# Kernel optimization log

Hardware: AMD Instinct MI355X
Metric: run time of the kernel (lower is better)

Reference implementation:

```python
import jax, jax.numpy as jnp
import numpy as np

B = 256          # graphs per batch
NN = 400         # ROI nodes per graph (N*(N-1)/2 = 79800 = input_dim)
HID = [32, 64, 128]
KS = [200, 100, 50]   # nodes kept after each TopKPooling (ratio 0.5 each)
EPS = 1e-5


def setup_inputs() -> dict:
    key = jax.random.key(0)
    ks = jax.random.split(key, 20)
    # flattened strict upper triangle of a nonnegative FC matrix per sample
    data = jax.random.uniform(ks[0], (B, NN * (NN - 1) // 2), dtype=jnp.float32)
    inp = {"data": data}
    dims = [1] + HID
    for l in range(3):
        fan_in = dims[l]
        inp[f"W{l+1}"] = jax.random.normal(ks[1 + 5 * l], (dims[l], dims[l + 1]), jnp.float32) / np.sqrt(fan_in)
        inp[f"b{l+1}"] = jnp.zeros((dims[l + 1],), jnp.float32)
        inp[f"g{l+1}"] = jnp.ones((dims[l + 1],), jnp.float32)      # BN gamma
        inp[f"be{l+1}"] = jnp.zeros((dims[l + 1],), jnp.float32)    # BN beta
        inp[f"p{l+1}"] = jax.random.normal(ks[4 + 5 * l], (dims[l + 1],), jnp.float32) * 0.1  # TopK score vector
    return inp


def _gcn_conv(A, X, W, b):
    # GCNConv with edge weights: add self loops (weight 1), symmetric D^-1/2 A D^-1/2
    n = A.shape[1]
    Al = A + jnp.eye(n, dtype=A.dtype)[None]          # (B, n, n)
    deg = Al.sum(axis=-1)                             # (B, n)
    dis = jnp.where(deg > 0, jax.lax.rsqrt(deg), 0.0)
    An = dis[:, :, None] * Al * dis[:, None, :]
    return jnp.einsum('bij,bjf->bif', An, X @ W) + b


def _block(A, X, W, b, g, be, p, k):
    # GCNConv -> ReLU -> BatchNorm(train stats) -> (dropout=identity) -> TopKPooling
    h = jax.nn.relu(_gcn_conv(A, X, W, b))
    mu = h.mean(axis=(0, 1))
    var = h.var(axis=(0, 1))
    h = (h - mu) * jax.lax.rsqrt(var + EPS) * g + be
    # TopKPooling: score = x . p / ||p||, keep top k per graph, gate by tanh(score)
    score = h @ p / jnp.linalg.norm(p)                # (B, n)
    vals, idx = jax.lax.top_k(score, k)               # (B, k)
    Xn = jnp.take_along_axis(h, idx[:, :, None], axis=1) * jnp.tanh(vals)[:, :, None]
    bi = jnp.arange(A.shape[0])[:, None, None]
    An = A[bi, idx[:, :, None], idx[:, None, :]]      # filter_adj: edges among kept nodes
    return An, Xn


def reference(data, W1, b1, g1, be1, p1, W2, b2, g2, be2, p2, W3, b3, g3, be3, p3):
    Bn = data.shape[0]
    iu0, iu1 = np.triu_indices(NN, 1)
    A = jnp.zeros((Bn, NN, NN), data.dtype).at[:, iu0, iu1].set(data)
    A = A + jnp.swapaxes(A, 1, 2)                     # symmetric FC adjacency, zero diag
    X = jnp.ones((Bn, NN, 1), data.dtype)             # initial node feature dim = 1
    A, X = _block(A, X, W1, b1, g1, be1, p1, KS[0])
    A, X = _block(A, X, W2, b2, g2, be2, p2, KS[1])
    A, X = _block(A, X, W3, b3, g3, be3, p3, KS[2])
    return X.max(axis=1)                              # global_max_pool -> (B, 128)
```

## Files before the change

kernel.cpp:

```cpp
#include <hip/hip_runtime.h>
#include <math.h>

#define BB   256
#define NN0  400
#define NE   79800
#define EPSF 1e-5f

__device__ __forceinline__ int tri_e(int a, int c) {
  return a*(NN0-1) - ((a*(a-1))>>1) + (c - a - 1);
}

__device__ __forceinline__ size_t PRI(int b, int ti, int tj, int r) {
  return (((size_t)b*7 + ti)*7 + tj)*64 + r;
}

__device__ __forceinline__ float wave_sum(float v) {
  #pragma unroll
  for (int o = 32; o > 0; o >>= 1) v += __shfl_xor(v, o, 64);
  return v;
}

__device__ __forceinline__ const float* lane0_ptr(const float* p) {
  uint64_t v = (uint64_t)p;
  uint32_t lo = (uint32_t)__builtin_amdgcn_readfirstlane((int)(v & 0xffffffffu));
  uint32_t hi = (uint32_t)__builtin_amdgcn_readfirstlane((int)(v >> 32));
  return (const float*)((((uint64_t)hi) << 32) | lo);
}

__device__ __forceinline__ void bitonic_desc(float* sc, int* si, int P) {
  const int tid = threadIdx.x;
  const int nt = blockDim.x;
  for (int k = 2; k <= P; k <<= 1) {
    for (int j = k >> 1; j > 0; j >>= 1) {
      __syncthreads();
      for (int i = tid; i < P; i += nt) {
        int ixj = i ^ j;
        if (ixj > i) {
          float a = sc[i], c = sc[ixj];
          int ai = si[i], ci = si[ixj];
          bool bef = (a > c) || (a == c && ai < ci);
          bool sw = ((i & k) == 0) ? !bef : bef;
          if (sw) { sc[i] = c; sc[ixj] = a; si[i] = ci; si[ixj] = ai; }
        }
      }
    }
  }
  __syncthreads();
}

__global__ __launch_bounds__(256) void k_tri_mv(
    const float* __restrict__ data,
    const float* __restrict__ pr_in, const float* __restrict__ pc_in,
    float* __restrict__ pr, float* __restrict__ pc) {
  __shared__ float tile[64][65];
  __shared__ float dI[64], dJ[64];
  const int xcd = blockIdx.x & 7, slot = blockIdx.x >> 3;
  const int b = xcd*32 + slot/7, q0 = slot % 7;
  const int tid = threadIdx.x;
  const int wave = tid >> 6, lane = tid & 63;
  const float* __restrict__ drow = data + (size_t)b*NE;
  int ti_a[4], tj_a[4];
  #pragma unroll
  for (int u = 0; u < 4; ++u) {
    int t = q0 + u*7;
    int ti = 0, rem = t;
    while (rem >= 7 - ti) { rem -= 7 - ti; ++ti; }
    ti_a[u] = ti; tj_a[u] = ti + rem;
  }
  float vreg[16];
  float rI = 0.f, rJ = 0.f;
  auto issue = [&](int u) {
    const int i0 = ti_a[u]*64, j0 = tj_a[u]*64;
    const int ni = min(64, NN0 - i0), nj = min(64, NN0 - j0);
    #pragma unroll
    for (int k = 0; k < 16; ++k) {
      const int rr = wave*16 + k;
      const int i = i0 + rr, j = j0 + lane;
      vreg[k] = 0.f;
      if (rr < ni && lane < nj && j > i) vreg[k] = drow[tri_e(i, j)];
    }
    if (pr_in) {
      if (tid < 64) {
        float a = 0.f;
        if (tid < ni) {
          const int tt = ti_a[u], r = tid;
          float acc = 1.f;
          for (int tj = tt; tj < 7; ++tj) acc += pr_in[PRI(b, tt, tj, r)];
          for (int ts = 0; ts <= tt; ++ts) acc += pc_in[PRI(b, ts, tt, r)];
          a = rsqrtf(acc);
        }
        rI = a;
      } else if (tid < 128) {
        const int c = tid - 64;
        float a = 0.f;
        if (c < nj) {
          const int tt = tj_a[u], r = c;
          float acc = 1.f;
          for (int tj = tt; tj < 7; ++tj) acc += pr_in[PRI(b, tt, tj, r)];
          for (int ts = 0; ts <= tt; ++ts) acc += pc_in[PRI(b, ts, tt, r)];
          a = rsqrtf(acc);
        }
        rJ = a;
      }
    } else {
      if (tid < 64) rI = (tid < ni) ? 1.f : 0.f;
      else if (tid < 128) rJ = (tid - 64 < nj) ? 1.f : 0.f;
    }
  };
  issue(0);
  #pragma unroll 1
  for (int u = 0; u < 4; ++u) {
    const int ti = ti_a[u], tj = tj_a[u];
    if (u) __syncthreads();
    #pragma unroll
    for (int k = 0; k < 16; ++k) tile[wave*16 + k][lane] = vreg[k];
    if (tid < 64) dI[tid] = rI;
    else if (tid < 128) dJ[tid-64] = rJ;
    __syncthreads();
    if (u + 1 < 4) issue(u + 1);
    {
      const int r = tid >> 2, q = tid & 3;
      float s = 0.f;
      #pragma unroll
      for (int c = 0; c < 16; ++c) s += tile[r][q*16 + c] * dJ[q*16 + c];
      s += __shfl_xor(s, 1, 64);
      s += __shfl_xor(s, 2, 64);
      if (q == 0) pr[PRI(b, ti, tj, r)] = s;
    }
    {
      const int c = tid >> 2, q = tid & 3;
      float s = 0.f;
      #pragma unroll
      for (int r = 0; r < 16; ++r) s += tile[q*16 + r][c] * dI[q*16 + r];
      s += __shfl_xor(s, 1, 64);
      s += __shfl_xor(s, 2, 64);
      if (q == 0) pc[PRI(b, ti, tj, c)] = s;
    }
  }
}

__global__ __launch_bounds__(256) void k_sfin_stats_red(
    const float* __restrict__ pr, const float* __restrict__ pc,
    const float* __restrict__ pr2, const float* __restrict__ pc2,
    const float* __restrict__ W1, const float* __restrict__ b1,
    float* __restrict__ s1, float* __restrict__ acc1) {
  __shared__ float sl[256];
  __shared__ float st[64];
  __shared__ float w1s[32], b1s[32];
  const int tid = threadIdx.x;
  const int i = blockIdx.x*256 + tid;
  if (tid < 32) { w1s[tid] = W1[tid]; b1s[tid] = b1[tid]; }
  if (tid < 64) st[tid] = 0.f;
  const int b = i / NN0, n = i % NN0;
  const int t = n >> 6, r = n & 63;
  float dacc = 1.f, sacc = 0.f;
  for (int tj = t; tj < 7; ++tj) { dacc += pr[PRI(b, t, tj, r)]; sacc += pr2[PRI(b, t, tj, r)]; }
  for (int ti = 0; ti <= t; ++ti) { dacc += pc[PRI(b, ti, t, r)]; sacc += pc2[PRI(b, ti, t, r)]; }
  const float d = rsqrtf(dacc);
  const float s = d * (d + sacc);
  s1[i] = s;
  sl[tid] = s;
  __syncthreads();
  const int f = tid & 31, sub = tid >> 5;
  const float w = w1s[f], bb = b1s[f];
  float S = 0.f, Q = 0.f;
  #pragma unroll
  for (int k = 0; k < 32; ++k) {
    const float ss = sl[sub*32 + k];
    const float h = fmaxf(ss*w + bb, 0.f);
    S += h; Q += h*h;
  }
  atomicAdd(&st[f], S);
  atomicAdd(&st[32+f], Q);
  __syncthreads();
  if (tid < 64) atomicAdd(&acc1[tid], st[tid]);
}

__global__ __launch_bounds__(512) void k_top1(
    const float* __restrict__ s1, const float* __restrict__ acc1,
    const float* __restrict__ W1, const float* __restrict__ b1,
    const float* __restrict__ g1, const float* __restrict__ be1,
    const float* __restrict__ p1, const float* __restrict__ W2,
    int* __restrict__ nodes2, int* __restrict__ sperm2, float* __restrict__ Y2) {
  __shared__ float sc[512]; __shared__ int si[512];
  __shared__ float sS[NN0];
  __shared__ float tvs[200];
  __shared__ int nds_l[200];
  __shared__ float w1s[32], b1s[32], cfs[32], scs[32], shs[32];
  __shared__ __align__(16) float hp[6400];
  __shared__ float c0s;
  const int tid = threadIdx.x;
  const int b = (blockIdx.x & 7)*32 + (blockIdx.x >> 3);
  if (tid < 32) { w1s[tid] = W1[tid]; b1s[tid] = b1[tid]; }
  if (tid < 64) {
    float scale = 0.f, shift = 0.f, pv = 0.f;
    if (tid < 32) {
      const float S = acc1[tid], Q = acc1[32 + tid];
      const float N = 102400.f;
      const float mu = S / N;
      const float var = Q / N - mu*mu;
      const float inv = rsqrtf(var + EPSF);
      scale = inv * g1[tid];
      shift = be1[tid] - mu * scale;
      pv = p1[tid];
    }
    const float pn = sqrtf(wave_sum(pv*pv));
    if (tid < 32) { scs[tid] = scale; shs[tid] = shift; cfs[tid] = scale*pv/pn; }
    float u = (tid < 32) ? shift*pv/pn : 0.f;
    u = wave_sum(u);
    if (tid == 0) c0s = u;
  }
  __syncthreads();
  const float c0 = c0s;
  {
    const int i = tid;
    if (i < NN0) {
      const float s = s1[(size_t)b*NN0 + i];
      sS[i] = s;
      float sco = c0;
      #pragma unroll
      for (int f = 0; f < 32; ++f) sco += fmaxf(s*w1s[f] + b1s[f], 0.f) * cfs[f];
      sc[i] = sco; si[i] = i;
    } else { sc[i] = -INFINITY; si[i] = 0x7fffffff; }
  }
  bitonic_desc(sc, si, 512);
  for (int k = tid; k < 200; k += 512) {
    tvs[k] = tanhf(sc[k]);
    nds_l[k] = si[k];
    nodes2[b*200 + k] = si[k];
  }
  __syncthreads();
  for (int o = tid; o < 6400; o += 512) {
    const int k = o >> 5, f = o & 31;
    const float s = sS[nds_l[k]];
    const float h = fmaxf(s*w1s[f] + b1s[f], 0.f);
    hp[o] = (h*scs[f] + shs[f]) * tvs[k];
  }
  __syncthreads();
  {
    const int g = tid & 63;
    float wr[32];
    #pragma unroll
    for (int f = 0; f < 32; ++f) wr[f] = W2[f*64 + g];
    for (int o = tid; o < 12800; o += 512) {
      const int k = o >> 6;
      float acc = 0.f;
      #pragma unroll
      for (int c4 = 0; c4 < 8; ++c4) {
        const float4 x4 = *(const float4*)&hp[(k<<5) + (c4<<2)];
        acc += x4.x*wr[c4*4] + x4.y*wr[c4*4+1] + x4.z*wr[c4*4+2] + x4.w*wr[c4*4+3];
      }
      Y2[(size_t)b*12800 + o] = acc;
    }
  }
  __syncthreads();
  if (tid < 256) {
    sc[tid] = (tid < 200) ? -(float)nds_l[tid] : -INFINITY;
    si[tid] = (tid < 200) ? tid : 0x7fffffff;
  }
  bitonic_desc(sc, si, 256);
  if (tid < 200) sperm2[b*200 + tid] = si[tid];
}

__global__ __launch_bounds__(256) void k_gatherA2(
    const float* __restrict__ data, const int* __restrict__ nodes2,
    const int* __restrict__ sperm2, float* __restrict__ A2, float* __restrict__ dis2) {
  __shared__ int nds[200], sp[200], sn[200];
  __shared__ float rowbuf[4][200];
  const int idx = blockIdx.x;
  const int r9 = idx >> 3;
  const int b = (idx & 7)*32 + r9/50;
  const int rg = r9 % 50;
  const int tid = threadIdx.x;
  if (tid < 200) { nds[tid] = nodes2[b*200 + tid]; sp[tid] = sperm2[b*200 + tid]; }
  __syncthreads();
  if (tid < 200) sn[tid] = nds[sp[tid]];
  __syncthreads();
  const int wave = tid >> 6, lane = tid & 63;
  const int i = rg*4 + wave;
  const int ni = nds[i];
  const float* __restrict__ drow = data + (size_t)b*NE;
  float accd = 0.f;
  for (int jj = lane; jj < 200; jj += 64) {
    const int sj = sn[jj];
    float v = 0.f;
    if (sj != ni) {
      const int a = min(ni, sj), c = max(ni, sj);
      v = drow[tri_e(a, c)];
    }
    rowbuf[wave][sp[jj]] = v;
    accd += v;
  }
  __syncthreads();
  accd = wave_sum(accd);
  const float dd = rsqrtf(1.f + accd);
  for (int j = lane; j < 200; j += 64)
    A2[((size_t)b*200 + i)*200 + j] = rowbuf[wave][j] * dd;
  if (lane == 0) dis2[b*200 + i] = dd;
}

__global__ __launch_bounds__(256) void k_conv2(
    const float* __restrict__ A2, const float* __restrict__ Y2,
    const float* __restrict__ dis2, const float* __restrict__ b2,
    float* __restrict__ h2g, float* __restrict__ acc2g) {
  __shared__ float dsb[200];
  __shared__ float st[128];
  const int tid = threadIdx.x;
  const int xcd = blockIdx.x & 7, slot = blockIdx.x >> 3;
  const int b = xcd*32 + slot/5, p = slot % 5;
  const int wave = tid >> 6, lane = tid & 63;
  if (tid < 128) st[tid] = 0.f;
  if (tid < 200) dsb[tid] = dis2[b*200 + tid];
  __syncthreads();
  const float bl = b2[lane];
  const int rb = p*40 + wave*10;
  const float* __restrict__ Yb = Y2 + (size_t)b*12800;
  const float* __restrict__ Aw = lane0_ptr(A2 + (size_t)b*40000 + rb);
  float acc[10];
  #pragma unroll
  for (int k = 0; k < 10; ++k) acc[k] = 0.f;
  float zA = Yb[lane], zB = Yb[64 + lane];
  #pragma unroll 2
  for (int jp = 0; jp < 100; ++jp) {
    const int j = jp << 1;
    const float za = zA, zb_ = zB;
    if (jp < 99) { zA = Yb[(j + 2)*64 + lane]; zB = Yb[(j + 3)*64 + lane]; }
    const float* __restrict__ Aj0 = Aw + (size_t)j*200;
    const float* __restrict__ Aj1 = Aw + (size_t)(j + 1)*200;
    #pragma unroll
    for (int k = 0; k < 10; ++k) acc[k] = fmaf(Aj0[k], za, acc[k]);
    #pragma unroll
    for (int k = 0; k < 10; ++k) acc[k] = fmaf(Aj1[k], zb_, acc[k]);
  }
  float ss = 0.f, qq = 0.f;
  #pragma unroll
  for (int k = 0; k < 10; ++k) {
    const int r = rb + k;
    const float d = dsb[r];
    const float y = Yb[(size_t)r*64 + lane];
    const float h = fmaxf(d*acc[k] + d*(d*y) + bl, 0.f);
    h2g[((size_t)b*200 + r)*64 + lane] = h;
    ss += h; qq += h*h;
  }
  atomicAdd(&st[lane], ss);
  atomicAdd(&st[64 + lane], qq);
  __syncthreads();
  if (tid < 128) atomicAdd(&acc2g[tid], st[tid]);
}

__global__ __launch_bounds__(512) void k_top2(
    const float* __restrict__ h2g, const float* __restrict__ acc2,
    const float* __restrict__ g2, const float* __restrict__ be2,
    const float* __restrict__ p2, const float* __restrict__ W3,
    const int* __restrict__ nodes2, int* __restrict__ nodes3,
    float* __restrict__ Y3) {
  __shared__ float sc[256]; __shared__ int si[256];
  __shared__ __align__(16) float xs[6400];
  __shared__ float sc2[64], sh2[64], cf2[64];
  __shared__ float c20s;
  const int tid = threadIdx.x;
  const int b = (blockIdx.x & 7)*32 + (blockIdx.x >> 3);
  if (tid < 64) {
    const float S = acc2[tid], Q = acc2[64 + tid];
    const float N = 51200.f;
    const float mu = S/N, var = Q/N - mu*mu, inv = rsqrtf(var + EPSF);
    const float scale = inv*g2[tid], shift = be2[tid] - mu*scale;
    const float pv = p2[tid];
    const float pn = sqrtf(wave_sum(pv*pv));
    sc2[tid] = scale; sh2[tid] = shift; cf2[tid] = scale*pv/pn;
    const float u = wave_sum(shift*pv/pn);
    if (tid == 0) c20s = u;
  }
  __syncthreads();
  const int wave = tid >> 6, lane = tid & 63;
  const float cf = cf2[lane];
  const float c20 = c20s;
  for (int i = wave; i < 200; i += 8) {
    float v = h2g[((size_t)b*200 + i)*64 + lane] * cf;
    v = wave_sum(v);
    if (lane == 0) { sc[i] = v + c20; si[i] = i; }
  }
  if (tid >= 200 && tid < 256) { sc[tid] = -INFINITY; si[tid] = 0x7fffffff; }
  bitonic_desc(sc, si, 256);
  const float scale = sc2[lane], shift = sh2[lane];
  for (int o = tid; o < 6400; o += 512) {
    const int k = o >> 6;
    const int idx = si[k];
    const float tv = tanhf(sc[k]);
    xs[o] = (h2g[((size_t)b*200 + idx)*64 + lane] * scale + shift) * tv;
  }
  for (int k = tid; k < 100; k += 512) nodes3[b*100 + k] = nodes2[b*200 + si[k]];
  __syncthreads();
  {
    const int g = tid & 127;
    float wr[64];
    #pragma unroll
    for (int f = 0; f < 64; ++f) wr[f] = W3[f*128 + g];
    for (int o = tid; o < 12800; o += 512) {
      const int k = o >> 7;
      float acc = 0.f;
      #pragma unroll
      for (int c4 = 0; c4 < 16; ++c4) {
        const float4 x4 = *(const float4*)&xs[(k<<6) + (c4<<2)];
        acc += x4.x*wr[c4*4] + x4.y*wr[c4*4+1] + x4.z*wr[c4*4+2] + x4.w*wr[c4*4+3];
      }
      Y3[(size_t)b*12800 + o] = acc;
    }
  }
}

__global__ __launch_bounds__(256) void k_gatherA3(
    const float* __restrict__ data, const int* __restrict__ nodes3,
    float* __restrict__ A3, float* __restrict__ dis3) {
  __shared__ int nds[100];
  const int slot = blockIdx.x >> 3;
  const int b = (blockIdx.x & 7)*32 + slot/25, rg = slot % 25;
  const int tid = threadIdx.x;
  if (tid < 100) nds[tid] = nodes3[b*100 + tid];
  __syncthreads();
  const int wave = tid >> 6, lane = tid & 63;
  const int i = rg*4 + wave;
  const int ni = nds[i];
  const float* __restrict__ drow = data + (size_t)b*NE;
  const int j0 = lane, j1 = 64 + lane;
  float v0 = 0.f, v1 = 0.f;
  if (j0 != i) {
    const int nj = nds[j0];
    const int a = min(ni, nj), c = max(ni, nj);
    v0 = drow[tri_e(a, c)];
  }
  if (j1 < 100 && j1 != i) {
    const int nj = nds[j1];
    const int a = min(ni, nj), c = max(ni, nj);
    v1 = drow[tri_e(a, c)];
  }
  const float accd = wave_sum(v0 + v1);
  const float dd = rsqrtf(1.f + accd);
  A3[((size_t)b*100 + i)*100 + j0] = v0 * dd;
  if (j1 < 100) A3[((size_t)b*100 + i)*100 + j1] = v1 * dd;
  if (lane == 0) dis3[b*100 + i] = dd;
}

__global__ __launch_bounds__(256) void k_conv3(
    const float* __restrict__ A3, const float* __restrict__ Y3,
    const float* __restrict__ dis3, const float* __restrict__ b3,
    float* __restrict__ h3g, float* __restrict__ acc3g) {
  __shared__ float dsb[100];
  __shared__ float st[256];
  const int tid = threadIdx.x;
  const int xcd = blockIdx.x & 7, slot = blockIdx.x >> 3;
  const int b = xcd*32 + slot/5, p = slot % 5;
  const int wave = tid >> 6, lane = tid & 63;
  st[tid] = 0.f;
  if (tid < 100) dsb[tid] = dis3[b*100 + tid];
  __syncthreads();
  const float bl0 = b3[lane], bl1 = b3[64 + lane];
  const int rb = p*20 + wave*5;
  const float* __restrict__ Yb = Y3 + (size_t)b*12800;
  const float* __restrict__ Aw = lane0_ptr(A3 + (size_t)b*10000 + rb);
  float ac0[5], ac1[5];
  #pragma unroll
  for (int k = 0; k < 5; ++k) { ac0[k] = 0.f; ac1[k] = 0.f; }
  float zA0 = Yb[lane],        zA1 = Yb[64 + lane];
  float zB0 = Yb[128 + lane],  zB1 = Yb[192 + lane];
  #pragma unroll 2
  for (int jp = 0; jp < 50; ++jp) {
    const int j = jp << 1;
    const float a0_ = zA0, a1_ = zA1, b0_ = zB0, b1_ = zB1;
    if (jp < 49) {
      zA0 = Yb[(j + 2)*128 + lane];  zA1 = Yb[(j + 2)*128 + 64 + lane];
      zB0 = Yb[(j + 3)*128 + lane];  zB1 = Yb[(j + 3)*128 + 64 + lane];
    }
    const float* __restrict__ Aj0 = Aw + (size_t)j*100;
    const float* __restrict__ Aj1 = Aw + (size_t)(j + 1)*100;
    #pragma unroll
    for (int k = 0; k < 5; ++k) {
      const float av = Aj0[k];
      ac0[k] = fmaf(av, a0_, ac0[k]);
      ac1[k] = fmaf(av, a1_, ac1[k]);
    }
    #pragma unroll
    for (int k = 0; k < 5; ++k) {
      const float av = Aj1[k];
      ac0[k] = fmaf(av, b0_, ac0[k]);
      ac1[k] = fmaf(av, b1_, ac1[k]);
    }
  }
  float ss0 = 0.f, qq0 = 0.f, ss1 = 0.f, qq1 = 0.f;
  #pragma unroll
  for (int k = 0; k < 5; ++k) {
    const int r = rb + k;
    const float d = dsb[r];
    const float y0 = Yb[(size_t)r*128 + lane];
    const float y1 = Yb[(size_t)r*128 + 64 + lane];
    const float h0 = fmaxf(d*ac0[k] + d*(d*y0) + bl0, 0.f);
    const float h1 = fmaxf(d*ac1[k] + d*(d*y1) + bl1, 0.f);
    h3g[((size_t)b*100 + r)*128 + lane] = h0;
    h3g[((size_t)b*100 + r)*128 + 64 + lane] = h1;
    ss0 += h0; qq0 += h0*h0; ss1 += h1; qq1 += h1*h1;
  }
  atomicAdd(&st[lane], ss0);
  atomicAdd(&st[64 + lane], ss1);
  atomicAdd(&st[128 + lane], qq0);
  atomicAdd(&st[192 + lane], qq1);
  __syncthreads();
  atomicAdd(&acc3g[tid], st[tid]);
}

__global__ __launch_bounds__(256) void k_top3(
    const float* __restrict__ h3g, const float* __restrict__ acc3,
    const float* __restrict__ g3, const float* __restrict__ be3,
    const float* __restrict__ p3, float* __restrict__ out) {
  __shared__ float sc[128]; __shared__ int si[128]; __shared__ float tv[64];
  __shared__ float scl[128], shl[128], cfl[128];
  __shared__ float red2[4];
  const int tid = threadIdx.x;
  const int b = (blockIdx.x & 7)*32 + (blockIdx.x >> 3);
  const int wave = tid >> 6, lane = tid & 63;
  float scale = 0.f, shift = 0.f, pv = 0.f;
  if (tid < 128) {
    const float S = acc3[tid], Q = acc3[128 + tid];
    const float N = 25600.f;
    const float mu = S/N, var = Q/N - mu*mu, inv = rsqrtf(var + EPSF);
    scale = inv*g3[tid]; shift = be3[tid] - mu*scale; pv = p3[tid];
    const float t2 = wave_sum(pv*pv);
    if (lane == 0) red2[wave] = t2;
  }
  __syncthreads();
  const float pn = sqrtf(red2[0] + red2[1]);
  if (tid < 128) {
    scl[tid] = scale; shl[tid] = shift; cfl[tid] = scale*pv/pn;
    const float u = wave_sum(shift*pv/pn);
    if (lane == 0) red2[2 + wave] = u;
  }
  __syncthreads();
  const float c30 = red2[2] + red2[3];
  const float clo = cfl[lane], chi = cfl[64 + lane];
  for (int i = wave; i < 100; i += 4) {
    const float* hr = h3g + ((size_t)b*100 + i)*128;
    float v = hr[lane]*clo + hr[64 + lane]*chi;
    v = wave_sum(v);
    if (lane == 0) { sc[i] = v + c30; si[i] = i; }
  }
  if (tid >= 100 && tid < 128) { sc[tid] = -INFINITY; si[tid] = 0x7fffffff; }
  bitonic_desc(sc, si, 128);
  if (tid < 50) tv[tid] = tanhf(sc[tid]);
  __syncthreads();
  if (tid < 128) {
    const float scalev = scl[tid], shiftv = shl[tid];
    float m = -INFINITY;
    for (int k = 0; k < 50; ++k) {
      const float h = h3g[((size_t)b*100 + si[k])*128 + tid];
      m = fmaxf(m, (h*scalev + shiftv)*tv[k]);
    }
    out[(size_t)b*128 + tid] = m;
  }
}

extern "C" void kernel_launch(void* const* d_in, const int* in_sizes, int n_in,
                              void* d_out, int out_size, void* d_ws, size_t ws_size,
                              hipStream_t stream) {
  (void)in_sizes; (void)n_in; (void)out_size; (void)ws_size;
  const float* data = (const float*)d_in[0];
  const float* W1 = (const float*)d_in[1];
  const float* b1 = (const float*)d_in[2];
  const float* g1 = (const float*)d_in[3];
  const float* be1 = (const float*)d_in[4];
  const float* p1 = (const float*)d_in[5];
  const float* W2 = (const float*)d_in[6];
  const float* b2 = (const float*)d_in[7];
  const float* g2 = (const float*)d_in[8];
  const float* be2 = (const float*)d_in[9];
  const float* p2 = (const float*)d_in[10];
  const float* W3 = (const float*)d_in[11];
  const float* b3 = (const float*)d_in[12];
  const float* g3 = (const float*)d_in[13];
  const float* be3 = (const float*)d_in[14];
  const float* p3 = (const float*)d_in[15];
  float* out = (float*)d_out;

  char* ws = (char*)d_ws;
  size_t off = 0;
  auto alloc = [&](size_t n) { size_t o = off; off += (n + 255) & ~(size_t)255; return o; };
  float* pr     = (float*)(ws + alloc((size_t)BB*49*64*4));
  float* pc     = (float*)(ws + alloc((size_t)BB*49*64*4));
  float* pr2    = (float*)(ws + alloc((size_t)BB*49*64*4));
  float* pc2    = (float*)(ws + alloc((size_t)BB*49*64*4));
  float* s1     = (float*)(ws + alloc((size_t)BB*NN0*4));
  float* accz   = (float*)(ws + alloc(448*4));
  int*   nodes2 = (int*)  (ws + alloc((size_t)BB*200*4));
  int*   sperm2 = (int*)  (ws + alloc((size_t)BB*200*4));
  float* Y2     = (float*)(ws + alloc((size_t)BB*12800*4));
  float* A2     = (float*)(ws + alloc((size_t)BB*40000*4));
  float* dis2   = (float*)(ws + alloc((size_t)BB*200*4));
  float* h2     = (float*)(ws + alloc((size_t)BB*12800*4));
  int*   nodes3 = (int*)  (ws + alloc((size_t)BB*100*4));
  float* Y3     = (float*)(ws + alloc((size_t)BB*12800*4));
  float* A3     = (float*)(ws + alloc((size_t)BB*10000*4));
  float* dis3   = (float*)(ws + alloc((size_t)BB*100*4));
  float* h3     = (float*)(ws + alloc((size_t)BB*12800*4));
  float* acc1 = accz;
  float* acc2 = accz + 64;
  float* acc3 = accz + 192;

  hipMemsetAsync(accz, 0, 448*4, stream);
  k_tri_mv<<<dim3(BB*7), dim3(256), 0, stream>>>(data, nullptr, nullptr, pr, pc);
  k_tri_mv<<<dim3(BB*7), dim3(256), 0, stream>>>(data, pr, pc, pr2, pc2);
  k_sfin_stats_red<<<dim3(400), dim3(256), 0, stream>>>(pr, pc, pr2, pc2, W1, b1, s1, acc1);
  k_top1<<<dim3(BB), dim3(512), 0, stream>>>(s1, acc1, W1, b1, g1, be1, p1, W2, nodes2, sperm2, Y2);
  k_gatherA2<<<dim3(BB*50), dim3(256), 0, stream>>>(data, nodes2, sperm2, A2, dis2);
  k_conv2<<<dim3(BB*5), dim3(256), 0, stream>>>(A2, Y2, dis2, b2, h2, acc2);
  k_top2<<<dim3(BB), dim3(512), 0, stream>>>(h2, acc2, g2, be2, p2, W3, nodes2, nodes3, Y3);
  k_gatherA3<<<dim3(BB*25), dim3(256), 0, stream>>>(data, nodes3, A3, dis3);
  k_conv3<<<dim3(BB*5), dim3(256), 0, stream>>>(A3, Y3, dis3, b3, h3, acc3);
  k_top3<<<dim3(BB), dim3(256), 0, stream>>>(h3, acc3, g3, be3, p3, out);
}
```

Measured before the change: 496.2 us.

## Restructure conv2/conv3 as LDS-staged 8x8 register-tiled batched matmuls

Both GCN conv kernels now use one block per graph instead of five. The adjacency tile is staged into shared memory: for conv2 it is double-buffered in 25-row chunks through register prefetch, and for conv3 the whole 100x100 matrix is loaded at once. Each thread then computes an 8x8 output tile with vectorized float4 loads, replacing scalar per-wave loads that read A through a uniform pointer. This raises arithmetic intensity and removes redundant reloads of Y, but cuts grid size to 256 blocks, idles some threads (tr>=25 or tr>=13), and uses 64 accumulator registers per thread, which may lower occupancy.

Result: faster. 446.9 us (-9.9%).

```diff
diff --git a/kernel.cpp b/kernel.cpp
--- a/kernel.cpp
+++ b/kernel.cpp
@@ -18,13 +18,6 @@
   #pragma unroll
   for (int o = 32; o > 0; o >>= 1) v += __shfl_xor(v, o, 64);
   return v;
-}
-
-__device__ __forceinline__ const float* lane0_ptr(const float* p) {
-  uint64_t v = (uint64_t)p;
-  uint32_t lo = (uint32_t)__builtin_amdgcn_readfirstlane((int)(v & 0xffffffffu));
-  uint32_t hi = (uint32_t)__builtin_amdgcn_readfirstlane((int)(v >> 32));
-  return (const float*)((((uint64_t)hi) << 32) | lo);
 }
 
 __device__ __forceinline__ void bitonic_desc(float* sc, int* si, int P) {
@@ -303,47 +296,100 @@
     const float* __restrict__ A2, const float* __restrict__ Y2,
     const float* __restrict__ dis2, const float* __restrict__ b2,
     float* __restrict__ h2g, float* __restrict__ acc2g) {
+  __shared__ __align__(16) float As[5000];
   __shared__ float dsb[200];
   __shared__ float st[128];
   const int tid = threadIdx.x;
-  const int xcd = blockIdx.x & 7, slot = blockIdx.x >> 3;
-  const int b = xcd*32 + slot/5, p = slot % 5;
-  const int wave = tid >> 6, lane = tid & 63;
+  const int b = (blockIdx.x & 7)*32 + (blockIdx.x >> 3);
+  const int tr = tid >> 3, tc = tid & 7;
   if (tid < 128) st[tid] = 0.f;
   if (tid < 200) dsb[tid] = dis2[b*200 + tid];
-  __syncthreads();
-  const float bl = b2[lane];
-  const int rb = p*40 + wave*10;
+  const float* __restrict__ Ab = A2 + (size_t)b*40000;
   const float* __restrict__ Yb = Y2 + (size_t)b*12800;
-  const float* __restrict__ Aw = lane0_ptr(A2 + (size_t)b*40000 + rb);
-  float acc[10];
+  float4 pf0, pf1, pf2, pf3;
+  float4 pf4 = make_float4(0.f, 0.f, 0.f, 0.f);
+  {
+    pf0 = *(const float4*)&Ab[(size_t)(tid)*4];
+    pf1 = *(const float4*)&Ab[(size_t)(tid + 256)*4];
+    pf2 = *(const float4*)&Ab[(size_t)(tid + 512)*4];
+    pf3 = *(const float4*)&Ab[(size_t)(tid + 768)*4];
+    if (tid < 226) pf4 = *(const float4*)&Ab[(size_t)(tid + 1024)*4];
+  }
+  *(float4*)&As[tid*4] = pf0;
+  *(float4*)&As[(tid + 256)*4] = pf1;
+  *(float4*)&As[(tid + 512)*4] = pf2;
+  *(float4*)&As[(tid + 768)*4] = pf3;
+  if (tid < 226) *(float4*)&As[(tid + 1024)*4] = pf4;
+  __syncthreads();
+  float acc[8][8];
   #pragma unroll
-  for (int k = 0; k < 10; ++k) acc[k] = 0.f;
-  float zA = Yb[lane], zB = Yb[64 + lane];
-  #pragma unroll 2
-  for (int jp = 0; jp < 100; ++jp) {
-    const int j = jp << 1;
-    const float za = zA, zb_ = zB;
-    if (jp < 99) { zA = Yb[(j + 2)*64 + lane]; zB = Yb[(j + 3)*64 + lane]; }
-    const float* __restrict__ Aj0 = Aw + (size_t)j*200;
-    const float* __restrict__ Aj1 = Aw + (size_t)(j + 1)*200;
-    #pragma unroll
-    for (int k = 0; k < 10; ++k) acc[k] = fmaf(Aj0[k], za, acc[k]);
-    #pragma unroll
-    for (int k = 0; k < 10; ++k) acc[k] = fmaf(Aj1[k], zb_, acc[k]);
-  }
-  float ss = 0.f, qq = 0.f;
-  #pragma unroll
-  for (int k = 0; k < 10; ++k) {
-    const int r = rb + k;
-    const float d = dsb[r];
-    const float y = Yb[(size_t)r*64 + lane];
-    const float h = fmaxf(d*acc[k] + d*(d*y) + bl, 0.f);
-    h2g[((size_t)b*200 + r)*64 + lane] = h;
-    ss += h; qq += h*h;
-  }
-  atomicAdd(&st[lane], ss);
-  atomicAdd(&st[64 + lane], qq);
+  for (int i = 0; i < 8; ++i)
+    #pragma unroll
+    for (int k = 0; k < 8; ++k) acc[i][k] = 0.f;
+  #pragma unroll 1
+  for (int c = 0; c < 8; ++c) {
+    if (c < 7) {
+      const float* __restrict__ src = Ab + (size_t)(c + 1)*5000;
+      pf0 = *(const float4*)&src[(size_t)(tid)*4];
+      pf1 = *(const float4*)&src[(size_t)(tid + 256)*4];
+      pf2 = *(const float4*)&src[(size_t)(tid + 512)*4];
+      pf3 = *(const float4*)&src[(size_t)(tid + 768)*4];
+      if (tid < 226) pf4 = *(const float4*)&src[(size_t)(tid + 1024)*4];
+    }
+    if (tr < 25) {
+      #pragma unroll 1
+      for (int js = 0; js < 25; ++js) {
+        const int j = c*25 + js;
+        float af[8], zf[8];
+        *(float4*)&af[0] = *(const float4*)&As[js*200 + tr*8];
+        *(float4*)&af[4] = *(const float4*)&As[js*200 + tr*8 + 4];
+        *(float4*)&zf[0] = *(const float4*)&Yb[(size_t)j*64 + tc*8];
+        *(float4*)&zf[4] = *(const float4*)&Yb[(size_t)j*64 + tc*8 + 4];
+        #pragma unroll
+        for (int i = 0; i < 8; ++i)
+          #pragma unroll
+          for (int k = 0; k < 8; ++k)
+            acc[i][k] = fmaf(af[i], zf[k], acc[i][k]);
+      }
+    }
+    __syncthreads();
+    if (c < 7) {
+      *(float4*)&As[tid*4] = pf0;
+      *(float4*)&As[(tid + 256)*4] = pf1;
+      *(float4*)&As[(tid + 512)*4] = pf2;
+      *(float4*)&As[(tid + 768)*4] = pf3;
+      if (tid < 226) *(float4*)&As[(tid + 1024)*4] = pf4;
+      __syncthreads();
+    }
+  }
+  if (tr < 25) {
+    float blv[8];
+    *(float4*)&blv[0] = *(const float4*)&b2[tc*8];
+    *(float4*)&blv[4] = *(const float4*)&b2[tc*8 + 4];
+    float ssl[8], qql[8];
+    #pragma unroll
+    for (int k = 0; k < 8; ++k) { ssl[k] = 0.f; qql[k] = 0.f; }
+    #pragma unroll
+    for (int i = 0; i < 8; ++i) {
+      const int r = tr*8 + i;
+      const float d = dsb[r];
+      float yv[8], hv[8];
+      *(float4*)&yv[0] = *(const float4*)&Yb[(size_t)r*64 + tc*8];
+      *(float4*)&yv[4] = *(const float4*)&Yb[(size_t)r*64 + tc*8 + 4];
+      #pragma unroll
+      for (int k = 0; k < 8; ++k) {
+        const float h = fmaxf(d*acc[i][k] + d*(d*yv[k]) + blv[k], 0.f);
+        hv[k] = h; ssl[k] += h; qql[k] += h*h;
+      }
+      *(float4*)&h2g[((size_t)b*200 + r)*64 + tc*8] = *(float4*)&hv[0];
+      *(float4*)&h2g[((size_t)b*200 + r)*64 + tc*8 + 4] = *(float4*)&hv[4];
+    }
+    #pragma unroll
+    for (int k = 0; k < 8; ++k) {
+      atomicAdd(&st[tc*8 + k], ssl[k]);
+      atomicAdd(&st[64 + tc*8 + k], qql[k]);
+    }
+  }
   __syncthreads();
   if (tid < 128) atomicAdd(&acc2g[tid], st[tid]);
 }
@@ -445,64 +491,67 @@
     const float* __restrict__ A3, const float* __restrict__ Y3,
     const float* __restrict__ dis3, const float* __restrict__ b3,
     float* __restrict__ h3g, float* __restrict__ acc3g) {
+  __shared__ __align__(16) float As[10016];
   __shared__ float dsb[100];
   __shared__ float st[256];
   const int tid = threadIdx.x;
-  const int xcd = blockIdx.x & 7, slot = blockIdx.x >> 3;
-  const int b = xcd*32 + slot/5, p = slot % 5;
-  const int wave = tid >> 6, lane = tid & 63;
+  const int b = (blockIdx.x & 7)*32 + (blockIdx.x >> 3);
+  const int tr = tid >> 4, tc = tid & 15;
   st[tid] = 0.f;
   if (tid < 100) dsb[tid] = dis3[b*100 + tid];
-  __syncthreads();
-  const float bl0 = b3[lane], bl1 = b3[64 + lane];
-  const int rb = p*20 + wave*5;
+  const float* __restrict__ Ab = A3 + (size_t)b*10000;
   const float* __restrict__ Yb = Y3 + (size_t)b*12800;
-  const float* __restrict__ Aw = lane0_ptr(A3 + (size_t)b*10000 + rb);
-  float ac0[5], ac1[5];
+  for (int t = tid; t < 2500; t += 256)
+    *(float4*)&As[t*4] = *(const float4*)&Ab[(size_t)t*4];
+  __syncthreads();
+  float acc[8][8];
   #pragma unroll
-  for (int k = 0; k < 5; ++k) { ac0[k] = 0.f; ac1[k] = 0.f; }
-  float zA0 = Yb[lane],        zA1 = Yb[64 + lane];
-  float zB0 = Yb[128 + lane],  zB1 = Yb[192 + lane];
-  #pragma unroll 2
-  for (int jp = 0; jp < 50; ++jp) {
-    const int j = jp << 1;
-    const float a0_ = zA0, a1_ = zA1, b0_ = zB0, b1_ = zB1;
-    if (jp < 49) {
-      zA0 = Yb[(j + 2)*128 + lane];  zA1 = Yb[(j + 2)*128 + 64 + lane];
-      zB0 = Yb[(j + 3)*128 + lane];  zB1 = Yb[(j + 3)*128 + 64 + lane];
-    }
-    const float* __restrict__ Aj0 = Aw + (size_t)j*100;
-    const float* __restrict__ Aj1 = Aw + (size_t)(j + 1)*100;
-    #pragma unroll
-    for (int k = 0; k < 5; ++k) {
-      const float av = Aj0[k];
-      ac0[k] = fmaf(av, a0_, ac0[k]);
-      ac1[k] = fmaf(av, a1_, ac1[k]);
-    }
-    #pragma unroll
-    for (int k = 0; k < 5; ++k) {
-      const float av = Aj1[k];
-      ac0[k] = fmaf(av, b0_, ac0[k]);
-      ac1[k] = fmaf(av, b1_, ac1[k]);
-    }
-  }
-  float ss0 = 0.f, qq0 = 0.f, ss1 = 0.f, qq1 = 0.f;
-  #pragma unroll
-  for (int k = 0; k < 5; ++k) {
-    const int r = rb + k;
-    const float d = dsb[r];
-    const float y0 = Yb[(size_t)r*128 + lane];
-    const float y1 = Yb[(size_t)r*128 + 64 + lane];
-    const float h0 = fmaxf(d*ac0[k] + d*(d*y0) + bl0, 0.f);
-    const float h1 = fmaxf(d*ac1[k] + d*(d*y1) + bl1, 0.f);
-    h3g[((size_t)b*100 + r)*128 + lane] = h0;
-    h3g[((size_t)b*100 + r)*128 + 64 + lane] = h1;
-    ss0 += h0; qq0 += h0*h0; ss1 += h1; qq1 += h1*h1;
-  }
-  atomicAdd(&st[lane], ss0);
-  atomicAdd(&st[64 + lane], ss1);
-  atomicAdd(&st[128 + lane], qq0);
-  atomicAdd(&st[192 + lane], qq1);
+  for (int i = 0; i < 8; ++i)
+    #pragma unroll
+    for (int k = 0; k < 8; ++k) acc[i][k] = 0.f;
+  if (tr < 13) {
+    #pragma unroll 2
+    for (int j = 0; j < 100; ++j) {
+      float af[8], zf[8];
+      *(float4*)&af[0] = *(const float4*)&As[j*100 + tr*8];
+      *(float4*)&af[4] = *(const float4*)&As[j*100 + tr*8 + 4];
+      *(float4*)&zf[0] = *(const float4*)&Yb[(size_t)j*128 + tc*8];
+      *(float4*)&zf[4] = *(const float4*)&Yb[(size_t)j*128 + tc*8 + 4];
+      #pragma unroll
+      for (int i = 0; i < 8; ++i)
+        #pragma unroll
+        for (int k = 0; k < 8; ++k)
+          acc[i][k] = fmaf(af[i], zf[k], acc[i][k]);
+    }
+    float blv[8];
+    *(float4*)&blv[0] = *(const float4*)&b3[tc*8];
+    *(float4*)&blv[4] = *(const float4*)&b3[tc*8 + 4];
+    float ssl[8], qql[8];
+    #pragma unroll
+    for (int k = 0; k < 8; ++k) { ssl[k] = 0.f; qql[k] = 0.f; }
+    #pragma unroll
+    for (int i = 0; i < 8; ++i) {
+      const int r = tr*8 + i;
+      if (r < 100) {
+        const float d = dsb[r];
+        float yv[8], hv[8];
+        *(float4*)&yv[0] = *(const float4*)&Yb[(size_t)r*128 + tc*8];
+        *(float4*)&yv[4] = *(const float4*)&Yb[(size_t)r*128 + tc*8 + 4];
+        #pragma unroll
+        for (int k = 0; k < 8; ++k) {
+          const float h = fmaxf(d*acc[i][k] + d*(d*yv[k]) + blv[k], 0.f);
+          hv[k] = h; ssl[k] += h; qql[k] += h*h;
+        }
+        *(float4*)&h3g[((size_t)b*100 + r)*128 + tc*8] = *(float4*)&hv[0];
+        *(float4*)&h3g[((size_t)b*100 + r)*128 + tc*8 + 4] = *(float4*)&hv[4];
+      }
+    }
+    #pragma unroll
+    for (int k = 0; k < 8; ++k) {
+      atomicAdd(&st[tc*8 + k], ssl[k]);
+      atomicAdd(&st[128 + tc*8 + k], qql[k]);
+    }
+  }
   __syncthreads();
   atomicAdd(&acc3g[tid], st[tid]);
 }
@@ -609,9 +658,9 @@
   k_sfin_stats_red<<<dim3(400), dim3(256), 0, stream>>>(pr, pc, pr2, pc2, W1, b1, s1, acc1);
   k_top1<<<dim3(BB), dim3(512), 0, stream>>>(s1, acc1, W1, b1, g1, be1, p1, W2, nodes2, sperm2, Y2);
   k_gatherA2<<<dim3(BB*50), dim3(256), 0, stream>>>(data, nodes2, sperm2, A2, dis2);
-  k_conv2<<<dim3(BB*5), dim3(256), 0, stream>>>(A2, Y2, dis2, b2, h2, acc2);
+  k_conv2<<<dim3(BB), dim3(256), 0, stream>>>(A2, Y2, dis2, b2, h2, acc2);
   k_top2<<<dim3(BB), dim3(512), 0, stream>>>(h2, acc2, g2, be2, p2, W3, nodes2, nodes3, Y3);
   k_gatherA3<<<dim3(BB*25), dim3(256), 0, stream>>>(data, nodes3, A3, dis3);
-  k_conv3<<<dim3(BB*5), dim3(256), 0, stream>>>(A3, Y3, dis3, b3, h3, acc3);
+  k_conv3<<<dim3(BB), dim3(256), 0, stream>>>(A3, Y3, dis3, b3, h3, acc3);
   k_top3<<<dim3(BB), dim3(256), 0, stream>>>(h3, acc3, g3, be3, p3, out);
 }
```
